# Optimization experiments

Hardware: AMD Instinct MI355X
Metric: run time of the kernel (lower is better)

The kernel has to match this reference:

```python
import jax, jax.numpy as jnp
import numpy as np


def _block_diag(blocks):
    """blocks: [K, m, n] -> dense block-diagonal [K*m, K*n] (vectorized scatter)."""
    K, m, n = blocks.shape
    out = jnp.zeros((K * m, K * n), blocks.dtype)
    r = jnp.arange(K)[:, None, None] * m + jnp.arange(m)[None, :, None]
    c = jnp.arange(K)[:, None, None] * n + jnp.arange(n)[None, None, :]
    return out.at[r, c].set(blocks)


def setup_inputs() -> dict:
    key = jax.random.key(0)
    k0, k1, k2, k3, k4 = jax.random.split(key, 5)
    n_state, n_input, T = 32, 16, 64
    n_all = n_state + n_input
    A = jax.random.normal(k0, (n_state, n_state), jnp.float32) * 0.3
    B = jax.random.normal(k1, (n_state, n_input), jnp.float32)
    M = jax.random.normal(k2, (T, n_all, n_all), jnp.float32)
    # symmetric PSD per-step cost blocks so the KKT matrix is invertible
    C = jnp.einsum('tij,tkj->tik', M, M) / n_all + 0.1 * jnp.eye(n_all, dtype=jnp.float32)
    c = jax.random.normal(k3, (T, n_all), jnp.float32)
    x0 = jax.random.normal(k4, (n_state,), jnp.float32)
    return {"A": A, "B": B, "C": C, "c": c, "T": T, "x0": x0}


def reference(A, B, C, c, T, x0):
    n_state = A.shape[0]
    n_input = B.shape[1]
    n_all = n_state + n_input

    # cost_mat = block_diag(C_0, ..., C_{T-1})  -> [n_all*T, n_all*T]
    cost_mat = _block_diag(C)

    # dynamics constraint matrix [n_state*T, n_all*T]
    AB = jnp.concatenate((A, B), axis=1)  # [n_state, n_all]
    AB_bd = _block_diag(jnp.broadcast_to(AB, (T - 1, n_state, n_all)) + jnp.zeros((T - 1, 1, 1), A.dtype))
    dynamics = jnp.zeros((n_state * T, n_all * T), A.dtype)
    dynamics = dynamics.at[:n_state, :n_state].set(jnp.eye(n_state, dtype=A.dtype))
    dynamics = dynamics.at[n_state:n_state * T, :n_all * (T - 1)].set(AB_bd)
    # -I coupling: rows n_state*t + i, cols n_all*t + i for t = 1..T-1
    rows = n_state * jnp.arange(1, T)[:, None] + jnp.arange(n_state)[None, :]
    cols = n_all * jnp.arange(1, T)[:, None] + jnp.arange(n_state)[None, :]
    dynamics = dynamics.at[rows, cols].set(-1.0)

    zero_mat = jnp.zeros((n_state * T, n_state * T), A.dtype)
    full_mat = jnp.block([[cost_mat, dynamics.T], [dynamics, zero_mat]])

    sol = jnp.zeros(n_all * T + n_state * T, A.dtype)
    sol = sol.at[n_all * T:n_all * T + n_state].set(x0)

    tau_mu = jnp.linalg.solve(full_mat, sol[:, None])[:, 0]
    tau_star = tau_mu[:n_all * T]
    mu_star = tau_mu[n_all * T:]
    return (tau_star, mu_star)
```

## Files before the change

kernel.cpp:

```cpp
#include <hip/hip_runtime.h>

#define NS 32
#define NI 16
#define NA 48
#define TT 64
#define HT 32

__launch_bounds__(256, 1)
__global__ void lqr_fast(const float* __restrict__ Ag,
                         const float* __restrict__ Bg,
                         const float* __restrict__ Cg,
                         const float* __restrict__ x0g,
                         float* __restrict__ out,
                         float* __restrict__ Kall,
                         float* __restrict__ Pall)
{
    __shared__ float  sXT[TT][NS];
    __shared__ double sA[NS][33];
    __shared__ double sB[NS][17];
    __shared__ double sP[NS][33];
    __shared__ double sPA[NS][33];
    __shared__ double sPB[NS][17];
    __shared__ double sHs[NI][33];
    __shared__ double sKt[NI][33];
    __shared__ double sGi[NI][17];
    __shared__ double sPp[NS][33];
    __shared__ double sx[2][NS];
    __shared__ double su[NI];

    const int tid  = threadIdx.x;
    const int wid  = tid >> 6, lane = tid & 63;
    const int pi   = tid >> 3, pj0 = (tid & 7) * 4, pb0 = (tid & 7) * 2;
    const int ki   = tid >> 4, kj0 = (tid & 15) * 2;

    for (int idx = tid; idx < NS * NS; idx += 256) {
        sA[idx >> 5][idx & 31] = (double)Ag[idx];
        sP[idx >> 5][idx & 31] = 0.0;
    }
    for (int idx = tid; idx < NS * NI; idx += 256) sB[idx >> 4][idx & 15] = (double)Bg[idx];
    __syncthreads();

    for (int t = TT - 1; t >= 0; --t) {
        const float* Ct = Cg + t * NA * NA;

        {
            double a0 = 0, a1 = 0, a2 = 0, a3 = 0, b0 = 0, b1 = 0;
            for (int k = 0; k < NS; ++k) {
                const double p = sP[pi][k];
                a0 += p * sA[k][pj0 + 0]; a1 += p * sA[k][pj0 + 1];
                a2 += p * sA[k][pj0 + 2]; a3 += p * sA[k][pj0 + 3];
                b0 += p * sB[k][pb0 + 0]; b1 += p * sB[k][pb0 + 1];
            }
            sPA[pi][pj0 + 0] = a0; sPA[pi][pj0 + 1] = a1;
            sPA[pi][pj0 + 2] = a2; sPA[pi][pj0 + 3] = a3;
            sPB[pi][pb0 + 0] = b0; sPB[pi][pb0 + 1] = b1;
        }
        __syncthreads();

        if (wid == 0) {
            const int ri = lane & 15, cg = lane >> 4, jb = cg * 4;
            double g0 = (double)Ct[(NS + ri) * NA + NS + jb + 0];
            double g1 = (double)Ct[(NS + ri) * NA + NS + jb + 1];
            double g2 = (double)Ct[(NS + ri) * NA + NS + jb + 2];
            double g3 = (double)Ct[(NS + ri) * NA + NS + jb + 3];
            for (int k = 0; k < NS; ++k) {
                const double b = sB[k][ri];
                g0 += b * sPB[k][jb + 0]; g1 += b * sPB[k][jb + 1];
                g2 += b * sPB[k][jb + 2]; g3 += b * sPB[k][jb + 3];
            }
#pragma unroll
            for (int k = 0; k < NI; ++k) {
                const double myslot = ((k & 3) == 0) ? g0 : ((k & 3) == 1) ? g1
                                     : ((k & 3) == 2) ? g2 : g3;
                const int    plv  = k + ((k >> 2) << 4);
                const double piv  = __shfl(myslot, plv, 64);
                const double cv   = __shfl(myslot, ri + ((k >> 2) << 4), 64);
                const double pr0  = __shfl(g0, k + (cg << 4), 64);
                const double pr1  = __shfl(g1, k + (cg << 4), 64);
                const double pr2  = __shfl(g2, k + (cg << 4), 64);
                const double pr3  = __shfl(g3, k + (cg << 4), 64);
                const double ip   = 1.0 / piv;
                const bool   rk   = (ri == k);
                g0 = rk ? ((jb + 0 == k) ? ip : pr0 * ip)
                        : ((jb + 0 == k) ? -cv * ip : g0 - cv * pr0 * ip);
                g1 = rk ? ((jb + 1 == k) ? ip : pr1 * ip)
                        : ((jb + 1 == k) ? -cv * ip : g1 - cv * pr1 * ip);
                g2 = rk ? ((jb + 2 == k) ? ip : pr2 * ip)
                        : ((jb + 2 == k) ? -cv * ip : g2 - cv * pr2 * ip);
                g3 = rk ? ((jb + 3 == k) ? ip : pr3 * ip)
                        : ((jb + 3 == k) ? -cv * ip : g3 - cv * pr3 * ip);
            }
            sGi[ri][jb + 0] = g0; sGi[ri][jb + 1] = g1;
            sGi[ri][jb + 2] = g2; sGi[ri][jb + 3] = g3;
        } else {
            const int e0 = tid - 64;
            for (int e = e0; e < NI * NS; e += 192) {
                const int i = e >> 5, j = e & 31;
                double acc = (double)Ct[j * NA + NS + i];
                for (int k = 0; k < NS; ++k) acc += sB[k][i] * sPA[k][j];
                sHs[i][j] = acc;
            }
            for (int e = e0; e < NS * NS; e += 192) {
                const int i = e >> 5, j = e & 31;
                double acc = (double)Ct[i * NA + j];
                for (int k = 0; k < NS; ++k) acc += sA[k][i] * sPA[k][j];
                sPp[i][j] = acc;
            }
        }
        __syncthreads();

        {
            double a0 = 0, a1 = 0;
            for (int k = 0; k < NI; ++k) {
                const double g = sGi[ki][k];
                a0 += g * sHs[k][kj0 + 0];
                a1 += g * sHs[k][kj0 + 1];
            }
            sKt[ki][kj0 + 0] = a0; sKt[ki][kj0 + 1] = a1;
            Kall[t * NI * NS + ki * NS + kj0 + 0] = (float)a0;
            Kall[t * NI * NS + ki * NS + kj0 + 1] = (float)a1;
        }
        __syncthreads();

        {
            double a0 = sPp[pi][pj0 + 0], a1 = sPp[pi][pj0 + 1];
            double a2 = sPp[pi][pj0 + 2], a3 = sPp[pi][pj0 + 3];
            for (int k = 0; k < NI; ++k) {
                const double h = sHs[k][pi];
                a0 -= h * sKt[k][pj0 + 0]; a1 -= h * sKt[k][pj0 + 1];
                a2 -= h * sKt[k][pj0 + 2]; a3 -= h * sKt[k][pj0 + 3];
            }
            double b0 = sPp[pj0 + 0][pi], b1 = sPp[pj0 + 1][pi];
            double b2 = sPp[pj0 + 2][pi], b3 = sPp[pj0 + 3][pi];
            for (int k = 0; k < NI; ++k) {
                const double hk = sKt[k][pi];
                b0 -= sHs[k][pj0 + 0] * hk; b1 -= sHs[k][pj0 + 1] * hk;
                b2 -= sHs[k][pj0 + 2] * hk; b3 -= sHs[k][pj0 + 3] * hk;
            }
            const double r0 = 0.5 * (a0 + b0), r1 = 0.5 * (a1 + b1);
            const double r2 = 0.5 * (a2 + b2), r3 = 0.5 * (a3 + b3);
            sP[pi][pj0 + 0] = r0; sP[pi][pj0 + 1] = r1;
            sP[pi][pj0 + 2] = r2; sP[pi][pj0 + 3] = r3;
            float* Pt = Pall + t * NS * NS + pi * NS + pj0;
            Pt[0] = (float)r0; Pt[1] = (float)r1; Pt[2] = (float)r2; Pt[3] = (float)r3;
        }
        __syncthreads();
    }

    if (tid < NS) sx[0][tid] = (double)x0g[tid];
    __syncthreads();
    int cur = 0;
    for (int t = 0; t < TT; ++t) {
        if (tid < NS) {
            const float xv = (float)sx[cur][tid];
            sXT[t][tid] = xv;
            out[t * NA + tid] = xv;
        } else if (tid >= 64 && tid < 64 + NI) {
            const int i = tid - 64;
            const float* Kt = Kall + t * NI * NS + i * NS;
            double acc = 0.0;
            for (int k = 0; k < NS; ++k) acc += (double)Kt[k] * sx[cur][k];
            su[i] = -acc;
            out[t * NA + NS + i] = (float)(-acc);
        }
        __syncthreads();
        if (t < TT - 1) {
            if (tid < NS) {
                double acc = 0.0;
                for (int k = 0; k < NS; ++k) acc += sA[tid][k] * sx[cur][k];
                for (int k = 0; k < NI; ++k) acc += sB[tid][k] * su[k];
                sx[cur ^ 1][tid] = acc;
            }
            __syncthreads();
            cur ^= 1;
        }
    }
    __syncthreads();

    for (int e = tid; e < TT * NS; e += 256) {
        const int t = e >> 5, i = e & 31;
        const float* Pt = Pall + t * NS * NS + i * NS;
        double acc = 0.0;
        for (int k = 0; k < NS; ++k) acc += (double)Pt[k] * (double)sXT[t][k];
        if (t == 0) acc = -acc;
        out[NA * TT + t * NS + i] = (float)acc;
    }
}

__launch_bounds__(256, 1)
__global__ void lqr_kernel_fb(const float* __restrict__ Ag,
                              const float* __restrict__ Bg,
                              const float* __restrict__ Cg,
                              const float* __restrict__ x0g,
                              float* __restrict__ out)
{
    __shared__ float  sKh[HT][NI][NS];
    __shared__ float  sXT[TT][NS];
    __shared__ double sA[NS][NS];
    __shared__ double sB[NS][NI];
    __shared__ double sP[NS][NS];
    __shared__ double sPA[NS][NS];
    __shared__ double sPB[NS][NI];
    __shared__ double sHs[NI][NS];
    __shared__ double sKt[NI][NS];
    __shared__ double sGi[NI][NI];
    __shared__ double sPp[NS][NS];
    __shared__ double sx[2][NS];
    __shared__ double su[NI];

    const int tid  = threadIdx.x;
    const int wid  = tid >> 6, lane = tid & 63;
    const int pi   = tid >> 3, pj0 = (tid & 7) * 4, pb0 = (tid & 7) * 2;
    const int ki   = tid >> 4, kj0 = (tid & 15) * 2;

    for (int idx = tid; idx < NS * NS; idx += 256) sA[idx >> 5][idx & 31] = (double)Ag[idx];
    for (int idx = tid; idx < NS * NI; idx += 256) sB[idx >> 4][idx & 15] = (double)Bg[idx];
    __syncthreads();

    auto step = [&](int t, bool storeK, int kbase, bool emitMu) {
        const float* Ct = Cg + t * NA * NA;
        {
            double a0 = 0, a1 = 0, a2 = 0, a3 = 0, b0 = 0, b1 = 0;
            for (int k = 0; k < NS; ++k) {
                const double p = sP[pi][k];
                a0 += p * sA[k][pj0 + 0]; a1 += p * sA[k][pj0 + 1];
                a2 += p * sA[k][pj0 + 2]; a3 += p * sA[k][pj0 + 3];
                b0 += p * sB[k][pb0 + 0]; b1 += p * sB[k][pb0 + 1];
            }
            sPA[pi][pj0 + 0] = a0; sPA[pi][pj0 + 1] = a1;
            sPA[pi][pj0 + 2] = a2; sPA[pi][pj0 + 3] = a3;
            sPB[pi][pb0 + 0] = b0; sPB[pi][pb0 + 1] = b1;
        }
        __syncthreads();
        if (wid == 0) {
            const int ri = lane & 15, cg = lane >> 4, jb = cg * 4;
            double g0 = (double)Ct[(NS + ri) * NA + NS + jb + 0];
            double g1 = (double)Ct[(NS + ri) * NA + NS + jb + 1];
            double g2 = (double)Ct[(NS + ri) * NA + NS + jb + 2];
            double g3 = (double)Ct[(NS + ri) * NA + NS + jb + 3];
            for (int k = 0; k < NS; ++k) {
                const double b = sB[k][ri];
                g0 += b * sPB[k][jb + 0]; g1 += b * sPB[k][jb + 1];
                g2 += b * sPB[k][jb + 2]; g3 += b * sPB[k][jb + 3];
            }
#pragma unroll
            for (int k = 0; k < NI; ++k) {
                const double myslot = ((k & 3) == 0) ? g0 : ((k & 3) == 1) ? g1
                                     : ((k & 3) == 2) ? g2 : g3;
                const int    plv  = k + ((k >> 2) << 4);
                const double piv  = __shfl(myslot, plv, 64);
                const double cv   = __shfl(myslot, ri + ((k >> 2) << 4), 64);
                const double pr0  = __shfl(g0, k + (cg << 4), 64);
                const double pr1  = __shfl(g1, k + (cg << 4), 64);
                const double pr2  = __shfl(g2, k + (cg << 4), 64);
                const double pr3  = __shfl(g3, k + (cg << 4), 64);
                const double ip   = 1.0 / piv;
                const bool   rk   = (ri == k);
                g0 = rk ? ((jb + 0 == k) ? ip : pr0 * ip)
                        : ((jb + 0 == k) ? -cv * ip : g0 - cv * pr0 * ip);
                g1 = rk ? ((jb + 1 == k) ? ip : pr1 * ip)
                        : ((jb + 1 == k) ? -cv * ip : g1 - cv * pr1 * ip);
                g2 = rk ? ((jb + 2 == k) ? ip : pr2 * ip)
                        : ((jb + 2 == k) ? -cv * ip : g2 - cv * pr2 * ip);
                g3 = rk ? ((jb + 3 == k) ? ip : pr3 * ip)
                        : ((jb + 3 == k) ? -cv * ip : g3 - cv * pr3 * ip);
            }
            sGi[ri][jb + 0] = g0; sGi[ri][jb + 1] = g1;
            sGi[ri][jb + 2] = g2; sGi[ri][jb + 3] = g3;
        } else {
            const int e0 = tid - 64;
            for (int e = e0; e < NI * NS; e += 192) {
                const int i = e >> 5, j = e & 31;
                double acc = (double)Ct[j * NA + NS + i];
                for (int k = 0; k < NS; ++k) acc += sB[k][i] * sPA[k][j];
                sHs[i][j] = acc;
            }
            for (int e = e0; e < NS * NS; e += 192) {
                const int i = e >> 5, j = e & 31;
                double acc = (double)Ct[i * NA + j];
                for (int k = 0; k < NS; ++k) acc += sA[k][i] * sPA[k][j];
                sPp[i][j] = acc;
            }
        }
        __syncthreads();
        {
            double a0 = 0, a1 = 0;
            for (int k = 0; k < NI; ++k) {
                const double g = sGi[ki][k];
                a0 += g * sHs[k][kj0 + 0];
                a1 += g * sHs[k][kj0 + 1];
            }
            sKt[ki][kj0 + 0] = a0; sKt[ki][kj0 + 1] = a1;
            if (storeK) {
                sKh[t - kbase][ki][kj0 + 0] = (float)a0;
                sKh[t - kbase][ki][kj0 + 1] = (float)a1;
            }
        }
        __syncthreads();
        {
            double a0 = sPp[pi][pj0 + 0], a1 = sPp[pi][pj0 + 1];
            double a2 = sPp[pi][pj0 + 2], a3 = sPp[pi][pj0 + 3];
            for (int k = 0; k < NI; ++k) {
                const double h = sHs[k][pi];
                a0 -= h * sKt[k][pj0 + 0]; a1 -= h * sKt[k][pj0 + 1];
                a2 -= h * sKt[k][pj0 + 2]; a3 -= h * sKt[k][pj0 + 3];
            }
            double b0 = sPp[pj0 + 0][pi], b1 = sPp[pj0 + 1][pi];
            double b2 = sPp[pj0 + 2][pi], b3 = sPp[pj0 + 3][pi];
            for (int k = 0; k < NI; ++k) {
                const double hk = sKt[k][pi];
                b0 -= sHs[k][pj0 + 0] * hk; b1 -= sHs[k][pj0 + 1] * hk;
                b2 -= sHs[k][pj0 + 2] * hk; b3 -= sHs[k][pj0 + 3] * hk;
            }
            sP[pi][pj0 + 0] = 0.5 * (a0 + b0); sP[pi][pj0 + 1] = 0.5 * (a1 + b1);
            sP[pi][pj0 + 2] = 0.5 * (a2 + b2); sP[pi][pj0 + 3] = 0.5 * (a3 + b3);
        }
        __syncthreads();
        if (emitMu && tid < NS) {
            double acc = 0.0;
            for (int k = 0; k < NS; ++k) acc += sP[tid][k] * (double)sXT[t][k];
            if (t == 0) acc = -acc;
            out[NA * TT + t * NS + tid] = (float)acc;
        }
    };

    auto sweep = [&](int tlo, int klo, int khi, bool emitMu) {
        for (int idx = tid; idx < NS * NS; idx += 256) sP[idx >> 5][idx & 31] = 0.0;
        __syncthreads();
        for (int t = TT - 1; t >= tlo; --t)
            step(t, (t >= klo && t < khi), klo, emitMu);
    };

    int cur = 0;
    auto forward = [&](int t0, int t1, int kbase) {
        for (int t = t0; t < t1; ++t) {
            if (tid < NS) {
                const float xv = (float)sx[cur][tid];
                sXT[t][tid] = xv;
                out[t * NA + tid] = xv;
            } else if (tid >= 64 && tid < 64 + NI) {
                const int i = tid - 64;
                double acc = 0.0;
                for (int k = 0; k < NS; ++k)
                    acc += (double)sKh[t - kbase][i][k] * sx[cur][k];
                su[i] = -acc;
                out[t * NA + NS + i] = (float)(-acc);
            }
            __syncthreads();
            if (t < TT - 1) {
                if (tid < NS) {
                    double acc = 0.0;
                    for (int k = 0; k < NS; ++k) acc += sA[tid][k] * sx[cur][k];
                    for (int k = 0; k < NI; ++k) acc += sB[tid][k] * su[k];
                    sx[cur ^ 1][tid] = acc;
                }
                __syncthreads();
                cur ^= 1;
            }
        }
    };

    sweep(0, 0, HT, false);
    if (tid < NS) sx[0][tid] = (double)x0g[tid];
    __syncthreads();
    forward(0, HT, 0);
    sweep(HT, HT, TT, false);
    forward(HT, TT, HT);
    sweep(0, 0, 0, true);
}

extern "C" void kernel_launch(void* const* d_in, const int* in_sizes, int n_in,
                              void* d_out, int out_size, void* d_ws, size_t ws_size,
                              hipStream_t stream) {
    const float *A = nullptr, *B = nullptr, *C = nullptr, *x0 = nullptr;
    for (int i = 0; i < n_in; ++i) {
        switch (in_sizes[i]) {
            case 1024:   A  = (const float*)d_in[i]; break;
            case 512:    B  = (const float*)d_in[i]; break;
            case 147456: C  = (const float*)d_in[i]; break;
            case 32:     x0 = (const float*)d_in[i]; break;
            default: break;
        }
    }
    if (!A || !B || !C || !x0) {
        A  = (const float*)d_in[0];
        B  = (const float*)d_in[1];
        C  = (const float*)d_in[2];
        x0 = (const float*)d_in[5];
    }

    const size_t need = (size_t)(TT * NI * NS + TT * NS * NS) * sizeof(float);
    if (d_ws != nullptr && ws_size >= need) {
        float* Kall = (float*)d_ws;
        float* Pall = Kall + TT * NI * NS;
        lqr_fast<<<1, 256, 0, stream>>>(A, B, C, x0, (float*)d_out, Kall, Pall);
    } else {
        lqr_kernel_fb<<<1, 256, 0, stream>>>(A, B, C, x0, (float*)d_out);
    }
}
```

Before: 585.9 us.

## Double-buffer per-step cost blocks in LDS, fast reciprocal, single-wave forward rollout

Each step's C_t block is prefetched from global memory into registers during the current step's compute, then written to a double-buffered LDS slot. This hides global-load latency on the serial Riccati recursion. The division in the 16x16 Gauss-Jordan inverse is replaced by a float reciprocal refined with two Newton iterations. The forward state rollout now runs in one wavefront using shuffles instead of block-wide barriers. Costs are extra LDS and registers, and a small numerical difference in the reciprocal.

Measured after the change: 614.4 us. +4.9%, slower.

```diff
diff --git a/kernel.cpp b/kernel.cpp
--- a/kernel.cpp
+++ b/kernel.cpp
@@ -5,6 +5,15 @@
 #define NA 48
 #define TT 64
 #define HT 32
+#define CSZ (NA * NA)
+#define C4  (CSZ / 4)
+
+__device__ __forceinline__ double fast_rcp(double x) {
+    double r = (double)(1.0f / (float)x);
+    r = r * (2.0 - x * r);
+    r = r * (2.0 - x * r);
+    return r;
+}
 
 __launch_bounds__(256, 1)
 __global__ void lqr_fast(const float* __restrict__ Ag,
@@ -15,6 +24,7 @@
                          float* __restrict__ Kall,
                          float* __restrict__ Pall)
 {
+    __shared__ float4 sC4[2][C4];
     __shared__ float  sXT[TT][NS];
     __shared__ double sA[NS][33];
     __shared__ double sB[NS][17];
@@ -25,8 +35,6 @@
     __shared__ double sKt[NI][33];
     __shared__ double sGi[NI][17];
     __shared__ double sPp[NS][33];
-    __shared__ double sx[2][NS];
-    __shared__ double su[NI];
 
     const int tid  = threadIdx.x;
     const int wid  = tid >> 6, lane = tid & 63;
@@ -38,10 +46,17 @@
         sP[idx >> 5][idx & 31] = 0.0;
     }
     for (int idx = tid; idx < NS * NI; idx += 256) sB[idx >> 4][idx & 15] = (double)Bg[idx];
+    {
+        const float4* src = (const float4*)(Cg + (TT - 1) * CSZ);
+        sC4[0][tid]       = src[tid];
+        sC4[0][tid + 256] = src[tid + 256];
+        if (tid < C4 - 512) sC4[0][tid + 512] = src[tid + 512];
+    }
     __syncthreads();
 
+    int cur = 0;
     for (int t = TT - 1; t >= 0; --t) {
-        const float* Ct = Cg + t * NA * NA;
+        const float* sCf = (const float*)sC4[cur];
 
         {
             double a0 = 0, a1 = 0, a2 = 0, a3 = 0, b0 = 0, b1 = 0;
@@ -57,12 +72,20 @@
         }
         __syncthreads();
 
+        float4 pf0 = {}, pf1 = {}, pf2 = {};
+        const bool doPf = (t > 0);
+        if (doPf) {
+            const float4* src = (const float4*)(Cg + (t - 1) * CSZ);
+            pf0 = src[tid];
+            pf1 = src[tid + 256];
+            if (tid >= 64 && tid < 128) pf2 = src[tid + 448];
+        }
+
         if (wid == 0) {
             const int ri = lane & 15, cg = lane >> 4, jb = cg * 4;
-            double g0 = (double)Ct[(NS + ri) * NA + NS + jb + 0];
-            double g1 = (double)Ct[(NS + ri) * NA + NS + jb + 1];
-            double g2 = (double)Ct[(NS + ri) * NA + NS + jb + 2];
-            double g3 = (double)Ct[(NS + ri) * NA + NS + jb + 3];
+            const float4 rv = *(const float4*)&sCf[(NS + ri) * NA + NS + jb];
+            double g0 = (double)rv.x, g1 = (double)rv.y;
+            double g2 = (double)rv.z, g3 = (double)rv.w;
             for (int k = 0; k < NS; ++k) {
                 const double b = sB[k][ri];
                 g0 += b * sPB[k][jb + 0]; g1 += b * sPB[k][jb + 1];
@@ -79,7 +102,7 @@
                 const double pr1  = __shfl(g1, k + (cg << 4), 64);
                 const double pr2  = __shfl(g2, k + (cg << 4), 64);
                 const double pr3  = __shfl(g3, k + (cg << 4), 64);
-                const double ip   = 1.0 / piv;
+                const double ip   = fast_rcp(piv);
                 const bool   rk   = (ri == k);
                 g0 = rk ? ((jb + 0 == k) ? ip : pr0 * ip)
                         : ((jb + 0 == k) ? -cv * ip : g0 - cv * pr0 * ip);
@@ -96,16 +119,23 @@
             const int e0 = tid - 64;
             for (int e = e0; e < NI * NS; e += 192) {
                 const int i = e >> 5, j = e & 31;
-                double acc = (double)Ct[j * NA + NS + i];
+                double acc = (double)sCf[j * NA + NS + i];
                 for (int k = 0; k < NS; ++k) acc += sB[k][i] * sPA[k][j];
                 sHs[i][j] = acc;
             }
             for (int e = e0; e < NS * NS; e += 192) {
                 const int i = e >> 5, j = e & 31;
-                double acc = (double)Ct[i * NA + j];
+                double acc = (double)sCf[i * NA + j];
                 for (int k = 0; k < NS; ++k) acc += sA[k][i] * sPA[k][j];
                 sPp[i][j] = acc;
             }
+        }
+
+        if (doPf) {
+            float4* dst = sC4[cur ^ 1];
+            dst[tid]       = pf0;
+            dst[tid + 256] = pf1;
+            if (tid >= 64 && tid < 128) dst[tid + 448] = pf2;
         }
         __syncthreads();
 
@@ -145,34 +175,39 @@
             Pt[0] = (float)r0; Pt[1] = (float)r1; Pt[2] = (float)r2; Pt[3] = (float)r3;
         }
         __syncthreads();
-    }
-
-    if (tid < NS) sx[0][tid] = (double)x0g[tid];
-    __syncthreads();
-    int cur = 0;
-    for (int t = 0; t < TT; ++t) {
-        if (tid < NS) {
-            const float xv = (float)sx[cur][tid];
-            sXT[t][tid] = xv;
-            out[t * NA + tid] = xv;
-        } else if (tid >= 64 && tid < 64 + NI) {
-            const int i = tid - 64;
-            const float* Kt = Kall + t * NI * NS + i * NS;
-            double acc = 0.0;
-            for (int k = 0; k < NS; ++k) acc += (double)Kt[k] * sx[cur][k];
-            su[i] = -acc;
-            out[t * NA + NS + i] = (float)(-acc);
-        }
-        __syncthreads();
-        if (t < TT - 1) {
-            if (tid < NS) {
-                double acc = 0.0;
-                for (int k = 0; k < NS; ++k) acc += sA[tid][k] * sx[cur][k];
-                for (int k = 0; k < NI; ++k) acc += sB[tid][k] * su[k];
-                sx[cur ^ 1][tid] = acc;
-            }
-            __syncthreads();
-            cur ^= 1;
+        cur ^= 1;
+    }
+
+    if (wid == 0) {
+        const int row = lane & 31;
+        double x = 0.0;
+        if (lane < NS) x = (double)x0g[lane];
+        for (int t = 0; t < TT; ++t) {
+            if (lane < NS) {
+                const float xv = (float)x;
+                sXT[t][lane] = xv;
+                out[t * NA + lane] = xv;
+            }
+            const float* Kt = Kall + t * NI * NS + (lane & 15) * NS;
+            double accU = 0.0;
+            for (int k = 0; k < NS; ++k) {
+                const double xk = __shfl(x, k, 64);
+                accU += (double)Kt[k] * xk;
+            }
+            const double u = -accU;
+            if (lane < NI) out[t * NA + NS + lane] = (float)u;
+            if (t < TT - 1) {
+                double accX = 0.0;
+                for (int k = 0; k < NS; ++k) {
+                    const double xk = __shfl(x, k, 64);
+                    accX += sA[row][k] * xk;
+                }
+                for (int k = 0; k < NI; ++k) {
+                    const double uk = __shfl(u, k, 64);
+                    accX += sB[row][k] * uk;
+                }
+                x = accX;
+            }
         }
     }
     __syncthreads();
```
